# Optimization experiments

Hardware: AMD Instinct MI355X
Metric: run time of the kernel (lower is better)

The kernel has to match this reference:

```python
import jax, jax.numpy as jnp
import numpy as np

N_NODES, N_EDGES, HID = 30000, 480000, 128
N_GRAPHS, N_CLASSES = 128, 6
BN_EPS, ADD_SCORE = 1e-5, 0.5


def setup_inputs():
    key = jax.random.key(0)
    ks = jax.random.split(key, 12)
    g = lambda i, shape: jax.random.normal(ks[i], shape, jnp.float32) * 0.05
    return dict(
        x=jax.random.normal(ks[0], (N_NODES, HID), jnp.float32),
        edge_index=jax.random.randint(ks[1], (2, N_EDGES), 0, N_NODES, jnp.int32),
        batch=jnp.sort(jax.random.randint(ks[2], (N_NODES,), 0, N_GRAPHS, jnp.int32)),
        Wl=g(3, (6, HID, HID)), bl=jnp.zeros((6, HID), jnp.float32),
        Wr=g(4, (6, HID, HID)),
        gamma=jnp.ones((6, HID), jnp.float32), beta=jnp.zeros((6, HID), jnp.float32),
        Wlin=g(5, (3, HID, 2 * HID)), blin=jnp.zeros((3, HID), jnp.float32),
        Wp=g(6, (3, 2 * HID)), bp=jnp.zeros((3,), jnp.float32),
        Wf1=g(7, (HID, HID)), bf1=jnp.zeros((HID,), jnp.float32),
        Wf2=g(8, (N_CLASSES, HID)), bf2=jnp.zeros((N_CLASSES,), jnp.float32),
    )


def _sage(x, src, dst, emf, Wl_i, bl_i, Wr_i, N):
    # PyG SAGEConv: lin_l(mean_{j->i} x_j) + lin_r(x_i); emf masks dead edges
    msg = x[src] * emf[:, None]                              # [E,H]
    s = jax.ops.segment_sum(msg, dst, num_segments=N)
    c = jax.ops.segment_sum(emf, dst, num_segments=N)
    mean = s / jnp.maximum(c, 1.0)[:, None]
    return mean @ Wl_i.T + bl_i + x @ Wr_i.T


def _bn(x, g, b, nvf):
    # training-mode BatchNorm over valid (non-merged-away) nodes only
    cnt = jnp.maximum(nvf.sum(), 1.0)
    mu = (x * nvf[:, None]).sum(0) / cnt
    var = (((x - mu) ** 2) * nvf[:, None]).sum(0) / cnt
    return g * (x - mu) * jax.lax.rsqrt(var + BN_EPS) + b


def _edge_pool(x, src, dst, emb, nvb, Wp_i, bp_i, N, E):
    h = x.shape[1]
    # raw edge score = Linear(cat(x[src], x[dst]))
    raw = (x @ Wp_i[:h])[src] + (x @ Wp_i[h:])[dst] + bp_i   # [E]
    neg = jnp.finfo(x.dtype).min
    mx = jax.ops.segment_max(jnp.where(emb, raw, neg), dst, num_segments=N)
    z = jnp.where(emb, jnp.exp(jnp.where(emb, raw - mx[dst], 0.0)), 0.0)
    den = jax.ops.segment_sum(z, dst, num_segments=N)
    score = z / jnp.maximum(den, 1e-16)[dst] + ADD_SCORE     # softmax per dst + 0.5

    # greedy edge matching in descending score order (sequential, int-only carry)
    order = jnp.argsort(-jnp.where(emb, jax.lax.stop_gradient(score), -jnp.inf))

    def step(carry, i):
        matched, cluster, chosen = carry
        s, t = src[i], dst[i]
        ok = emb[i] & (~matched[s]) & (~matched[t]) & (s != t)
        rep, oth = jnp.minimum(s, t), jnp.maximum(s, t)
        matched = matched.at[s].set(matched[s] | ok)
        matched = matched.at[t].set(matched[t] | ok)
        cluster = cluster.at[oth].set(jnp.where(ok, rep, cluster[oth]))
        chosen = chosen.at[rep].set(jnp.where(ok, i, chosen[rep]))
        return (matched, cluster, chosen), None

    init = (~nvb, jnp.arange(N, dtype=jnp.int32), jnp.full((N,), -1, jnp.int32))
    (matched, cluster, chosen), _ = jax.lax.scan(step, init, order)

    # merged node = (x_s + x_t) * score(chosen edge); singleton score = 1
    nscore = jnp.where(chosen >= 0, score[jnp.maximum(chosen, 0)], 1.0)
    new_x = jax.ops.segment_sum(x, cluster, num_segments=N) * nscore[:, None]
    nvb2 = nvb & (cluster == jnp.arange(N, dtype=jnp.int32))
    # remap edges to cluster representatives; coalesce duplicates (self-loops kept, as PyG)
    key = jnp.where(emb, cluster[src] * N + cluster[dst], -1)  # N*N < 2**31
    uk = jnp.unique(key, size=E, fill_value=-1)
    emb2 = uk >= 0
    ukc = jnp.maximum(uk, 0)
    return new_x, ukc // N, ukc % N, emb2, nvb2


def reference(x, edge_index, batch, Wl, bl, Wr, gamma, beta, Wlin, blin, Wp, bp, Wf1, bf1, Wf2, bf2):
    N, E = x.shape[0], edge_index.shape[1]
    src, dst = edge_index[0], edge_index[1]
    emb = jnp.ones((E,), bool)   # edge-valid mask (fixed-shape graph coarsening)
    nvb = jnp.ones((N,), bool)   # node-valid mask
    for blk in range(3):
        emf, nvf = emb.astype(x.dtype), nvb.astype(x.dtype)
        i = 2 * blk
        h = _bn(jax.nn.relu(_sage(x, src, dst, emf, Wl[i], bl[i], Wr[i], N)), gamma[i], beta[i], nvf)
        h2 = _bn(jax.nn.relu(_sage(h, src, dst, emf, Wl[i + 1], bl[i + 1], Wr[i + 1], N)), gamma[i + 1], beta[i + 1], nvf)
        x = jnp.concatenate([h2, h], axis=1) @ Wlin[blk].T + blin[blk]  # dropout = identity (eval)
        x, src, dst, emb, nvb = _edge_pool(x, src, dst, emb, nvb, Wp[blk], bp[blk], N, E)
    nvf = nvb.astype(x.dtype)
    sums = jax.ops.segment_sum(x * nvf[:, None], batch, num_segments=N_GRAPHS)
    cnt = jax.ops.segment_sum(nvf, batch, num_segments=N_GRAPHS)
    pooled = sums / jnp.maximum(cnt, 1.0)[:, None]           # global_mean_pool
    hfc = jax.nn.relu(pooled @ Wf1.T + bf1)
    return jax.nn.log_softmax(hfc @ Wf2.T + bf2, axis=1)
```

## Files before the change

kernel.cpp:

```cpp
#include <hip/hip_runtime.h>
#include <stdint.h>

#define NN 30000
#define NE 480000
#define HID 128
#define NG 128
#define NC 6
#define BN_EPS 1e-5f
#define WPB 938
#define SLOTS 4

typedef unsigned int u32;
typedef unsigned long long u64;

__device__ __forceinline__ u64 ent_key(int4 ent) {
  return ((u64)(u32)ent.y << 32) | (u32)ent.x;
}

__global__ void k_init(const int* __restrict__ ei, int* srcA, int* dstA, int* nvb,
                       int* scal, int* b3, int* i2, float* gbuf) {
  int t = blockIdx.x * 256 + threadIdx.x;
  if (t < NE) { srcA[t] = ei[t]; dstA[t] = ei[NE + t]; }
  if (t < NN) nvb[t] = 1;
  if (t < 2 * NN) { b3[t] = 0; i2[t] = 0; }
  if (t < NG * HID + NG) gbuf[t] = 0.f;
  if (t == 0) { scal[0] = NE; scal[1] = 0; }
}

__global__ void k_csr_count(const int* __restrict__ pE, const int* __restrict__ src,
                            const int* __restrict__ dst, int* __restrict__ cnt,
                            int* __restrict__ icnt, const int* __restrict__ nvb,
                            int* __restrict__ pcnt) {
  int t = blockIdx.x * 256 + threadIdx.x;
  if (t < NN && nvb[t]) atomicAdd(pcnt, 1);
  if (t < *pE) {
    int s = src[t], d = dst[t];
    atomicAdd(&cnt[d], 1);
    if (s != d) { atomicAdd(&icnt[s], 1); atomicAdd(&icnt[d], 1); }
  }
}

__global__ __launch_bounds__(1024) void k_scan2(const int* __restrict__ in0, int* __restrict__ out0,
                                                const int* __restrict__ in1, int* __restrict__ out1) {
  const int* in = blockIdx.x ? in1 : in0;
  int* out = blockIdx.x ? out1 : out0;
  __shared__ int part[1024];
  int t = threadIdx.x;
  int chunk = (NN + 1023) / 1024;
  int b = t * chunk, e = b + chunk;
  if (b > NN) b = NN;
  if (e > NN) e = NN;
  int s = 0;
  for (int i = b; i < e; i++) s += in[i];
  part[t] = s;
  __syncthreads();
  for (int off = 1; off < 1024; off <<= 1) {
    int v = (t >= off) ? part[t - off] : 0;
    __syncthreads();
    part[t] += v;
    __syncthreads();
  }
  int excl = (t == 0) ? 0 : part[t - 1];
  for (int i = b; i < e; i++) { out[i] = excl; excl += in[i]; }
  if (t == 0) out[NN] = part[1023];
}

__global__ void k_csr_scatter(const int* __restrict__ pE, const int* __restrict__ dst,
                              const int* __restrict__ coff, int* __restrict__ cursor,
                              int* __restrict__ eids) {
  int e = blockIdx.x * 256 + threadIdx.x;
  if (e >= *pE) return;
  int d = dst[e];
  int pos = coff[d] + atomicAdd(&cursor[d], 1);
  eids[pos] = e;
}

__global__ __launch_bounds__(256) void k_sage_gather(
    const int* __restrict__ coff, const int* __restrict__ eids,
    const int* __restrict__ src, const float* __restrict__ x,
    float* __restrict__ mean) {
  int grp = threadIdx.x >> 5;
  int lane = threadIdx.x & 31;
  int n = blockIdx.x * 8 + grp;
  if (n >= NN) return;
  int b = coff[n], e2 = coff[n + 1];
  float4 acc = make_float4(0.f, 0.f, 0.f, 0.f);
  for (int i = b; i < e2; i++) {
    int s = src[eids[i]];
    float4 v = *(const float4*)(x + (size_t)s * HID + lane * 4);
    acc.x += v.x; acc.y += v.y; acc.z += v.z; acc.w += v.w;
  }
  float inv = 1.0f / fmaxf((float)(e2 - b), 1.0f);
  acc.x *= inv; acc.y *= inv; acc.z *= inv; acc.w *= inv;
  *(float4*)(mean + (size_t)n * HID + lane * 4) = acc;
}

__global__ __launch_bounds__(256) void gemm_dual(
    const float* __restrict__ A1, const float* __restrict__ W1,
    const float* __restrict__ A2, const float* __restrict__ W2,
    const float* __restrict__ bias, float* __restrict__ out,
    int M, int ldw, int relu, double* __restrict__ bnsum) {
  if (blockIdx.x == 0 && threadIdx.x < 2 * HID) bnsum[threadIdx.x] = 0.0;
  __shared__ float As[64][33];
  __shared__ float Ws[32][132];
  int row0 = blockIdx.x * 64;
  int tid = threadIdx.x;
  int cid = tid & 31;
  int rid = tid >> 5;
  float acc[8][4];
#pragma unroll
  for (int r = 0; r < 8; r++)
#pragma unroll
    for (int c = 0; c < 4; c++) acc[r][c] = 0.f;

  for (int srcI = 0; srcI < 2; ++srcI) {
    const float* A = srcI ? A2 : A1;
    const float* W = srcI ? W2 : W1;
    for (int kc = 0; kc < 128; kc += 32) {
#pragma unroll
      for (int i = 0; i < 2; ++i) {
        int idx = tid + i * 256;
        int r = idx >> 3;
        int c4 = (idx & 7) << 2;
        int gr = row0 + r;
        float4 v = make_float4(0.f, 0.f, 0.f, 0.f);
        if (gr < M) v = *(const float4*)(A + (size_t)gr * 128 + kc + c4);
        As[r][c4 + 0] = v.x; As[r][c4 + 1] = v.y; As[r][c4 + 2] = v.z; As[r][c4 + 3] = v.w;
      }
#pragma unroll
      for (int i = 0; i < 4; ++i) {
        int idx = tid + i * 256;
        int j = idx >> 3;
        int c4 = (idx & 7) << 2;
        float4 v = *(const float4*)(W + (size_t)j * ldw + kc + c4);
        Ws[c4 + 0][j] = v.x; Ws[c4 + 1][j] = v.y; Ws[c4 + 2][j] = v.z; Ws[c4 + 3][j] = v.w;
      }
      __syncthreads();
#pragma unroll
      for (int kk = 0; kk < 32; ++kk) {
        float4 w = *(const float4*)(&Ws[kk][cid * 4]);
#pragma unroll
        for (int r = 0; r < 8; ++r) {
          float a = As[rid * 8 + r][kk];
          acc[r][0] += a * w.x; acc[r][1] += a * w.y; acc[r][2] += a * w.z; acc[r][3] += a * w.w;
        }
      }
      __syncthreads();
    }
  }
#pragma unroll
  for (int r = 0; r < 8; ++r) {
    int gr = row0 + rid * 8 + r;
    if (gr >= M) continue;
#pragma unroll
    for (int c = 0; c < 4; ++c) {
      float v = acc[r][c] + bias[cid * 4 + c];
      if (relu) v = fmaxf(v, 0.f);
      out[(size_t)gr * 128 + cid * 4 + c] = v;
    }
  }
}

__global__ __launch_bounds__(128) void k_bn_stats(const float* __restrict__ x,
                                                  const int* __restrict__ nvb,
                                                  double* __restrict__ sums) {
  int k = threadIdx.x;
  int n0 = blockIdx.x * 64;
  float s = 0.f, q = 0.f;
  for (int r = 0; r < 64; r++) {
    int n = n0 + r;
    if (n >= NN) break;
    if (!nvb[n]) continue;
    float v = x[(size_t)n * HID + k];
    s += v; q += v * v;
  }
  atomicAdd(&sums[k], (double)s);
  atomicAdd(&sums[HID + k], (double)q);
}

__global__ void k_bn_apply(float* __restrict__ x, const double* __restrict__ sums,
                           const int* __restrict__ cnt, const float* __restrict__ gamma,
                           const float* __restrict__ beta) {
  int t = blockIdx.x * 256 + threadIdx.x;
  if (t >= NN * HID) return;
  int k = t & 127;
  double c = (double)((*cnt > 1) ? *cnt : 1);
  double mu = sums[k] / c;
  double var = sums[HID + k] / c - mu * mu;
  if (var < 0.0) var = 0.0;
  float inv = (float)(1.0 / sqrt(var + (double)BN_EPS));
  x[t] = gamma[k] * (x[t] - (float)mu) * inv + beta[k];
}

__global__ void k_node_proj(const float* __restrict__ x, const float* __restrict__ Wp,
                            float* __restrict__ px1, float* __restrict__ px2) {
  int n = blockIdx.x * 256 + threadIdx.x;
  if (n >= NN) return;
  const float* xr = x + (size_t)n * HID;
  float s1 = 0.f, s2 = 0.f;
#pragma unroll 8
  for (int k = 0; k < HID; k += 4) {
    float4 v = *(const float4*)(xr + k);
    float4 w1 = *(const float4*)(Wp + k);
    float4 w2 = *(const float4*)(Wp + HID + k);
    s1 += v.x * w1.x + v.y * w1.y + v.z * w1.z + v.w * w1.w;
    s2 += v.x * w2.x + v.y * w2.y + v.z * w2.z + v.w * w2.w;
  }
  px1[n] = s1; px2[n] = s2;
}

__global__ void k_edge_softmax_seed(
    const int* __restrict__ coff, const int* __restrict__ eids,
    const int* __restrict__ src, const float* __restrict__ px1,
    const float* __restrict__ px2, const float* __restrict__ bp,
    float* __restrict__ score, u64* __restrict__ ekey, u64* __restrict__ S) {
  int n = blockIdx.x * 256 + threadIdx.x;
  if (n >= NN) return;
  S[n] = 0ull;
  int b = coff[n], e2 = coff[n + 1];
  if (b == e2) return;
  float p2 = px2[n] + *bp;
  float mx = -3.4e38f;
  for (int i = b; i < e2; i++) {
    float r = px1[src[eids[i]]] + p2;
    mx = fmaxf(mx, r);
  }
  double den = 0.0;
  for (int i = b; i < e2; i++) {
    int eid = eids[i];
    float z = expf(px1[src[eid]] + p2 - mx);
    score[eid] = z;
    den += (double)z;
  }
  if (den < 1e-16) den = 1e-16;
  double invd = 1.0 / den;
  for (int i = b; i < e2; i++) {
    int eid = eids[i];
    float sc = (float)((double)score[eid] * invd) + 0.5f;
    score[eid] = sc;
    ekey[eid] = ((u64)__float_as_uint(sc) << 32) | (u64)(0xFFFFFFFFu - (u32)eid);
  }
}

__global__ void k_inc_scatter(const int* __restrict__ pE, const int* __restrict__ src,
                              const int* __restrict__ dst, const u64* __restrict__ ekey,
                              const int* __restrict__ ioff, int* __restrict__ icur,
                              int4* __restrict__ ielist) {
  int e = blockIdx.x * 256 + threadIdx.x;
  if (e >= *pE) return;
  int s = src[e], d = dst[e];
  if (s == d) return;
  u64 k = ekey[e];
  int4 ent;
  ent.x = (int)(u32)(k & 0xFFFFFFFFull);
  ent.y = (int)(u32)(k >> 32);
  ent.w = 0;
  ent.z = d;
  ielist[ioff[s] + atomicAdd(&icur[s], 1)] = ent;
  ent.z = s;
  ielist[ioff[d] + atomicAdd(&icur[d], 1)] = ent;
}

__global__ __launch_bounds__(256) void k_suitor(
    const int* __restrict__ ioff, const int4* __restrict__ ielist,
    const int* __restrict__ src, const int* __restrict__ dst,
    u64* __restrict__ S) {
  int wid = threadIdx.x >> 6;
  int lane = threadIdx.x & 63;
  int n = blockIdx.x * 4 + wid;
  if (n >= NN) return;
  int cur = n;
  while (cur >= 0) {
    int b = ioff[cur], e2 = ioff[cur + 1];
    int deg = e2 - b;
    if (deg == 0) break;
    if (deg <= 64 * SLOTS) {
      u64 key[SLOTS]; int pv[SLOTS];
#pragma unroll
      for (int s = 0; s < SLOTS; s++) {
        key[s] = 0; pv[s] = 0;
        int i = b + s * 64 + lane;
        if (i < e2) {
          int4 ent = ielist[i];
          key[s] = ent_key(ent);
          pv[s] = ent.z;
        }
      }
      long long res;
      for (;;) {
        u64 localBest = 0;
#pragma unroll
        for (int s = 0; s < SLOTS; s++) {
          if (!key[s]) continue;
          u64 sv = __hip_atomic_load(&S[pv[s]], __ATOMIC_RELAXED, __HIP_MEMORY_SCOPE_AGENT);
          if (sv >= key[s]) key[s] = 0;
          else if (key[s] > localBest) localBest = key[s];
        }
        u64 bestKey = localBest;
#pragma unroll
        for (int o = 32; o > 0; o >>= 1) {
          u64 other = __shfl_xor(bestKey, o, 64);
          if (other > bestKey) bestKey = other;
        }
        if (bestKey == 0) { res = -1; break; }
        int ms = -1;
#pragma unroll
        for (int s = 0; s < SLOTS; s++)
          if (ms < 0 && key[s] == bestKey) ms = s;
        u64 ball = __ballot(ms >= 0);
        int owner = (int)(__ffsll((long long)ball) - 1);
        long long r0 = -3;
        if (lane == owner) {
          int bv = pv[ms];
          u64 old = atomicMax(&S[bv], bestKey);
          if (old >= bestKey) { key[ms] = 0; r0 = -2; }
          else if (old == 0) r0 = -1;
          else {
            int eo = (int)(0xFFFFFFFFu - (u32)(old & 0xFFFFFFFFull));
            int so = src[eo], do_ = dst[eo];
            r0 = (so == bv) ? do_ : so;
          }
        }
        res = __shfl(r0, owner, 64);
        if (res != -2) break;
      }
      if (res < 0) break;
      cur = (int)res;
    } else {
      u64 bestKey = 0;
      for (int i = b + lane; i < e2; i += 64) {
        int4 ent = ielist[i];
        u64 k = ent_key(ent);
        if (k <= bestKey) continue;
        u64 sv = __hip_atomic_load(&S[ent.z], __ATOMIC_RELAXED, __HIP_MEMORY_SCOPE_AGENT);
        if (k > sv) bestKey = k;
      }
#pragma unroll
      for (int o = 32; o > 0; o >>= 1) {
        u64 other = __shfl_xor(bestKey, o, 64);
        if (other > bestKey) bestKey = other;
      }
      long long r0 = -1;
      if (bestKey != 0 && lane == 0) {
        int e = (int)(0xFFFFFFFFu - (u32)(bestKey & 0xFFFFFFFFull));
        int es = src[e], ed = dst[e];
        int bv = (es == cur) ? ed : es;
        u64 old = atomicMax(&S[bv], bestKey);
        if (old >= bestKey) r0 = cur;
        else if (old != 0) {
          int eo = (int)(0xFFFFFFFFu - (u32)(old & 0xFFFFFFFFull));
          int so = src[eo], do_ = dst[eo];
          r0 = (so == bv) ? do_ : so;
        }
      }
      long long res = (bestKey != 0) ? __shfl(r0, 0, 64) : -1;
      cur = (int)res;
    }
  }
}

__global__ __launch_bounds__(256) void k_new_x(
    const u64* __restrict__ S, const int* __restrict__ src, const int* __restrict__ dst,
    const float* __restrict__ score, const float* __restrict__ x,
    float* __restrict__ out, int* __restrict__ cluster,
    int* __restrict__ nvb, int* __restrict__ b3zero) {
  int gt = blockIdx.x * 256 + threadIdx.x;
  if (gt < 2 * NN) b3zero[gt] = 0;
  int grp = threadIdx.x >> 5;
  int lane = threadIdx.x & 31;
  int n = blockIdx.x * 8 + grp;
  if (n >= NN) return;
  u64 k = S[n];
  int partner = -1;
  int rep = n;
  bool isOth = false;
  float sc = 1.f;
  if (k) {
    int e = (int)(0xFFFFFFFFu - (u32)(k & 0xFFFFFFFFull));
    int s = src[e], d = dst[e];
    int other = (s == n) ? d : s;
    if (S[other] == k) {
      if (n > other) { isOth = true; rep = other; }
      else { partner = other; sc = score[e]; }
    }
  }
  float4 v = make_float4(0.f, 0.f, 0.f, 0.f);
  if (!isOth) {
    v = *(const float4*)(x + (size_t)n * HID + lane * 4);
    if (partner >= 0) {
      float4 w = *(const float4*)(x + (size_t)partner * HID + lane * 4);
      v.x = (v.x + w.x) * sc; v.y = (v.y + w.y) * sc;
      v.z = (v.z + w.z) * sc; v.w = (v.w + w.w) * sc;
    }
  }
  *(float4*)(out + (size_t)n * HID + lane * 4) = v;
  if (lane == 0) {
    cluster[n] = rep;
    nvb[n] = (nvb[n] && !isOth) ? 1 : 0;
  }
}

__global__ void k_bucket_count(const int* __restrict__ pE, const int* __restrict__ src,
                               const int* __restrict__ cluster, int* __restrict__ bcount) {
  int e = blockIdx.x * 256 + threadIdx.x;
  if (e >= *pE) return;
  atomicAdd(&bcount[cluster[src[e]]], 1);
}

__global__ __launch_bounds__(1024) void k_scan(const int* __restrict__ in, int* __restrict__ out,
                                               int n, int* totalDst) {
  __shared__ int part[1024];
  int t = threadIdx.x;
  int chunk = (n + 1023) / 1024;
  int b = t * chunk, e = b + chunk;
  if (b > n) b = n;
  if (e > n) e = n;
  int s = 0;
  for (int i = b; i < e; i++) s += in[i];
  part[t] = s;
  __syncthreads();
  for (int off = 1; off < 1024; off <<= 1) {
    int v = (t >= off) ? part[t - off] : 0;
    __syncthreads();
    part[t] += v;
    __syncthreads();
  }
  int excl = (t == 0) ? 0 : part[t - 1];
  int total = part[1023];
  for (int i = b; i < e; i++) { out[i] = excl; excl += in[i]; }
  if (t == 0) {
    out[n] = total;
    if (totalDst) *totalDst = total;
  }
}

__global__ void k_bucket_scatter(const int* __restrict__ pE, const int* __restrict__ src,
                                 const int* __restrict__ dst, const int* __restrict__ cluster,
                                 const int* __restrict__ boffs, int* __restrict__ bcursor,
                                 int* __restrict__ bucket) {
  int e = blockIdx.x * 256 + threadIdx.x;
  if (e >= *pE) return;
  int cs = cluster[src[e]], cd = cluster[dst[e]];
  int pos = boffs[cs] + atomicAdd(&bcursor[cs], 1);
  bucket[pos] = cd;
}

__global__ __launch_bounds__(256) void k_dedup_bitmap(
    const int* __restrict__ boffs, int* __restrict__ bucket,
    int* __restrict__ ucount) {
  __shared__ u32 bm[4][960];
  int wid = threadIdx.x >> 6;
  int lane = threadIdx.x & 63;
  int n = blockIdx.x * 4 + wid;
  int b = boffs[n], e = boffs[n + 1];
  for (int w = lane; w < 960; w += 64) bm[wid][w] = 0;
  __syncthreads();
  for (int i = b + lane; i < e; i += 64)
    atomicOr(&bm[wid][bucket[i] >> 5], 1u << (bucket[i] & 31));
  __syncthreads();
  int w0 = lane * 15;
  int w1 = w0 + 15; if (w1 > WPB) w1 = WPB;
  int cnt = 0;
  for (int w = w0; w < w1; w++) cnt += __popc(bm[wid][w]);
  int inc = cnt;
  for (int o = 1; o < 64; o <<= 1) { int v = __shfl_up(inc, o); if (lane >= o) inc += v; }
  int excl = inc - cnt;
  int total = __shfl(inc, 63);
  int pos = b + excl;
  for (int w = w0; w < w1; w++) {
    u32 v = bm[wid][w];
    while (v) { int bit = __ffs(v) - 1; bucket[pos++] = (w << 5) | bit; v &= v - 1; }
  }
  if (lane == 0) ucount[n] = total;
}

__global__ void k_emit(const int* __restrict__ boffs, const int* __restrict__ bucket,
                       const int* __restrict__ bucount, const int* __restrict__ bnoffs,
                       int* __restrict__ srcO, int* __restrict__ dstO,
                       int* __restrict__ b3zero, int* __restrict__ i2zero,
                       int* __restrict__ pcnt) {
  int t = blockIdx.x * 256 + threadIdx.x;
  int stride = gridDim.x * 256;
  for (int z = t; z < 2 * NN; z += stride) { b3zero[z] = 0; i2zero[z] = 0; }
  if (t == 0) *pcnt = 0;
  if (t >= NN) return;
  int u = bucount[t], b = boffs[t], o = bnoffs[t];
  for (int i = 0; i < u; i++) { srcO[o + i] = t; dstO[o + i] = bucket[b + i]; }
}

__global__ void k_graph_pool(const int* __restrict__ nvb, const int* __restrict__ batch,
                             const float* __restrict__ x, float* __restrict__ gsum,
                             float* __restrict__ gcnt) {
  int t = blockIdx.x * 256 + threadIdx.x;
  int n = t >> 2;
  if (n >= NN) return;
  if (!nvb[n]) return;
  int sub = t & 3;
  int g = batch[n];
  const float* xr = x + (size_t)n * HID + sub * 32;
  float* o = gsum + (size_t)g * HID + sub * 32;
#pragma unroll
  for (int i = 0; i < 8; i++) {
    float4 v = *(const float4*)(xr + i * 4);
    atomicAdd(o + i * 4 + 0, v.x); atomicAdd(o + i * 4 + 1, v.y);
    atomicAdd(o + i * 4 + 2, v.z); atomicAdd(o + i * 4 + 3, v.w);
  }
  if (sub == 0) atomicAdd(&gcnt[g], 1.0f);
}

__global__ __launch_bounds__(128) void k_head1(const float* __restrict__ gsum,
                                               const float* __restrict__ gcnt,
                                               const float* __restrict__ Wf1,
                                               const float* __restrict__ bf1,
                                               float* __restrict__ hfc) {
  int g = blockIdx.x;
  int j = threadIdx.x;
  __shared__ float p[HID];
  float c = fmaxf(gcnt[g], 1.f);
  p[j] = gsum[g * HID + j] / c;
  __syncthreads();
  float s = bf1[j];
  const float* w = Wf1 + (size_t)j * HID;
  for (int k = 0; k < HID; k++) s += p[k] * w[k];
  hfc[g * HID + j] = fmaxf(s, 0.f);
}

__global__ void k_head2(const float* __restrict__ hfc, const float* __restrict__ Wf2,
                        const float* __restrict__ bf2, float* __restrict__ out) {
  int g = blockIdx.x;
  int t = threadIdx.x;
  __shared__ float lg[NC];
  if (t < NC) {
    float s = bf2[t];
    const float* w = Wf2 + (size_t)t * HID;
    const float* h = hfc + (size_t)g * HID;
    for (int k = 0; k < HID; k++) s += h[k] * w[k];
    lg[t] = s;
  }
  __syncthreads();
  if (t == 0) {
    float m = lg[0];
    for (int c = 1; c < NC; c++) m = fmaxf(m, lg[c]);
    float se = 0.f;
    for (int c = 0; c < NC; c++) se += expf(lg[c] - m);
    float lse = m + logf(se);
    for (int c = 0; c < NC; c++) out[g * NC + c] = lg[c] - lse;
  }
}

extern "C" void kernel_launch(void* const* d_in, const int* in_sizes, int n_in,
                              void* d_out, int out_size, void* d_ws, size_t ws_size,
                              hipStream_t stream) {
  const float* x0 = (const float*)d_in[0];
  const int* ei = (const int*)d_in[1];
  const int* batch = (const int*)d_in[2];
  const float* Wl = (const float*)d_in[3];
  const float* bl = (const float*)d_in[4];
  const float* Wr = (const float*)d_in[5];
  const float* gamma = (const float*)d_in[6];
  const float* beta = (const float*)d_in[7];
  const float* Wlin = (const float*)d_in[8];
  const float* blin = (const float*)d_in[9];
  const float* Wp = (const float*)d_in[10];
  const float* bp = (const float*)d_in[11];
  const float* Wf1 = (const float*)d_in[12];
  const float* bf1 = (const float*)d_in[13];
  const float* Wf2 = (const float*)d_in[14];
  const float* bf2 = (const float*)d_in[15];
  float* out = (float*)d_out;

  const int NH = NN * HID;
  size_t off = 0;
  char* base = (char*)d_ws;
  auto carve = [&](size_t bytes) -> char* {
    char* p = base + off;
    off += (bytes + 255) & ~(size_t)255;
    return p;
  };
  float* xa = (float*)carve((size_t)NH * 4);
  float* xb = (float*)carve((size_t)NH * 4);
  float* xc = (float*)carve((size_t)NH * 4);
  float* xd = (float*)carve((size_t)NH * 4);
  int* srcA = (int*)carve((size_t)NE * 4);
  int* dstA = (int*)carve((size_t)NE * 4);
  int* srcB = (int*)carve((size_t)NE * 4);
  int* dstB = (int*)carve((size_t)NE * 4);
  float* escore = (float*)carve((size_t)NE * 4);
  int* ebucket = (int*)carve((size_t)NE * 4);
  int* eids = (int*)carve((size_t)NE * 4);
  u64* ekey = (u64*)carve((size_t)NE * 8);
  u64* S = (u64*)carve((size_t)NN * 8);
  float* npx1 = (float*)carve((size_t)NN * 4);
  float* npx2 = (float*)carve((size_t)NN * 4);
  int* ncluster = (int*)carve((size_t)NN * 4);
  int* nvb = (int*)carve((size_t)NN * 4);
  int* b3 = (int*)carve((size_t)3 * NN * 4);
  int* bcount = b3;
  int* bcursor = b3 + NN;
  int* bucount = b3 + 2 * NN;
  int* i2 = (int*)carve((size_t)2 * NN * 4);
  int* icnt = i2;
  int* icursor = i2 + NN;
  int* boffs = (int*)carve((size_t)(NN + 1) * 4);
  int* bnoffs = (int*)carve((size_t)(NN + 1) * 4);
  int* csroff = (int*)carve((size_t)(NN + 1) * 4);
  int* ioff = (int*)carve((size_t)(NN + 1) * 4);
  double* bnsum = (double*)carve((size_t)2 * HID * 8);
  float* gbuf = (float*)carve((size_t)(NG * HID + NG) * 4);
  float* gsum = gbuf;
  float* gcnt = gbuf + NG * HID;
  float* ghfc = (float*)carve((size_t)NG * HID * 4);
  int* scal = (int*)carve(64 * 4);
  (void)ws_size; (void)n_in; (void)in_sizes; (void)out_size;

  int4* ielist = (int4*)xc;

  int* pE = scal;
  int* pcnt = scal + 1;

  hipMemcpyAsync(xa, x0, (size_t)NH * 4, hipMemcpyDeviceToDevice, stream);
  k_init<<<1875, 256, 0, stream>>>(ei, srcA, dstA, nvb, scal, b3, i2, gbuf);

  int* srcC = srcA; int* dstC = dstA; int* srcN = srcB; int* dstN = dstB;
  float* xcur = xa;
  float* xtmp = xd;

  auto sage = [&](const float* xin, float* xout, int L) {
    k_sage_gather<<<3750, 256, 0, stream>>>(csroff, eids, srcC, xin, xtmp);
    gemm_dual<<<469, 256, 0, stream>>>(xtmp, Wl + (size_t)L * HID * HID, xin,
                                       Wr + (size_t)L * HID * HID, bl + (size_t)L * HID,
                                       xout, NN, HID, 1, bnsum);
    k_bn_stats<<<469, 128, 0, stream>>>(xout, nvb, bnsum);
    k_bn_apply<<<15000, 256, 0, stream>>>(xout, bnsum, pcnt, gamma + (size_t)L * HID,
                                          beta + (size_t)L * HID);
  };

  for (int b = 0; b < 3; b++) {
    k_csr_count<<<1875, 256, 0, stream>>>(pE, srcC, dstC, bcount, icnt, nvb, pcnt);
    k_scan2<<<2, 1024, 0, stream>>>(bcount, csroff, icnt, ioff);
    k_csr_scatter<<<1875, 256, 0, stream>>>(pE, dstC, csroff, bcursor, eids);

    sage(xcur, xb, 2 * b);
    sage(xb, xc, 2 * b + 1);
    gemm_dual<<<469, 256, 0, stream>>>(xc, Wlin + (size_t)b * HID * 2 * HID, xb,
                                       Wlin + (size_t)b * HID * 2 * HID + HID,
                                       blin + (size_t)b * HID, xcur, NN, 2 * HID, 0, bnsum);

    k_node_proj<<<118, 256, 0, stream>>>(xcur, Wp + (size_t)b * 2 * HID, npx1, npx2);
    k_edge_softmax_seed<<<118, 256, 0, stream>>>(csroff, eids, srcC, npx1, npx2, bp + b,
                                                 escore, ekey, S);
    k_inc_scatter<<<1875, 256, 0, stream>>>(pE, srcC, dstC, ekey, ioff, icursor, ielist);
    k_suitor<<<7500, 256, 0, stream>>>(ioff, ielist, srcC, dstC, S);
    k_new_x<<<3750, 256, 0, stream>>>(S, srcC, dstC, escore, xcur, xtmp,
                                      ncluster, nvb, b3);

    if (b < 2) {
      k_bucket_count<<<1875, 256, 0, stream>>>(pE, srcC, ncluster, bcount);
      k_scan<<<1, 1024, 0, stream>>>(bcount, boffs, NN, (int*)nullptr);
      k_bucket_scatter<<<1875, 256, 0, stream>>>(pE, srcC, dstC, ncluster, boffs, bcursor,
                                                 ebucket);
      k_dedup_bitmap<<<7500, 256, 0, stream>>>(boffs, ebucket, bucount);
      k_scan<<<1, 1024, 0, stream>>>(bucount, bnoffs, NN, pE);
      k_emit<<<235, 256, 0, stream>>>(boffs, ebucket, bucount, bnoffs, srcN, dstN,
                                      b3, i2, pcnt);
      { int* t = srcC; srcC = srcN; srcN = t; t = dstC; dstC = dstN; dstN = t; }
    }
    { float* t = xcur; xcur = xtmp; xtmp = t; }
  }

  k_graph_pool<<<469, 256, 0, stream>>>(nvb, batch, xcur, gsum, gcnt);
  k_head1<<<NG, 128, 0, stream>>>(gsum, gcnt, Wf1, bf1, ghfc);
  k_head2<<<NG, 32, 0, stream>>>(ghfc, Wf2, bf2, out);
}
```

Baseline: 2.843 ms.

## Fuse BN stats into 128x128 GEMM, pre-gather CSR sources, drop input copy

The GEMM is retiled to 128-row blocks with an 8x8 register tile per thread. It now accumulates per-column batch-norm sums in its epilogue, so the separate stats kernel is gone. The CSR scatter also writes source node ids in CSR order, which removes the eids indirection in the SAGE gather and the edge softmax; the gather is unrolled by two. The initial device-to-device copy of x is replaced by reading the input directly in the first block. These changes cut kernel launches and memory passes, at the cost of more register pressure in the GEMM and fewer blocks launched.

```diff
diff --git a/kernel.cpp b/kernel.cpp
--- a/kernel.cpp
+++ b/kernel.cpp
@@ -9,6 +9,7 @@
 #define BN_EPS 1e-5f
 #define WPB 938
 #define SLOTS 4
+#define GPAD 132
 
 typedef unsigned int u32;
 typedef unsigned long long u64;
@@ -65,117 +66,131 @@
   if (t == 0) out[NN] = part[1023];
 }
 
-__global__ void k_csr_scatter(const int* __restrict__ pE, const int* __restrict__ dst,
-                              const int* __restrict__ coff, int* __restrict__ cursor,
-                              int* __restrict__ eids) {
+__global__ void k_csr_scatter(const int* __restrict__ pE, const int* __restrict__ src,
+                              const int* __restrict__ dst, const int* __restrict__ coff,
+                              int* __restrict__ cursor, int* __restrict__ eids,
+                              int* __restrict__ gsrc) {
   int e = blockIdx.x * 256 + threadIdx.x;
   if (e >= *pE) return;
   int d = dst[e];
   int pos = coff[d] + atomicAdd(&cursor[d], 1);
   eids[pos] = e;
+  gsrc[pos] = src[e];
 }
 
 __global__ __launch_bounds__(256) void k_sage_gather(
-    const int* __restrict__ coff, const int* __restrict__ eids,
-    const int* __restrict__ src, const float* __restrict__ x,
-    float* __restrict__ mean) {
+    const int* __restrict__ coff, const int* __restrict__ gsrc,
+    const float* __restrict__ x, float* __restrict__ mean,
+    double* __restrict__ bnsum) {
+  if (blockIdx.x == 0 && threadIdx.x < 2 * HID) bnsum[threadIdx.x] = 0.0;
   int grp = threadIdx.x >> 5;
   int lane = threadIdx.x & 31;
   int n = blockIdx.x * 8 + grp;
   if (n >= NN) return;
   int b = coff[n], e2 = coff[n + 1];
   float4 acc = make_float4(0.f, 0.f, 0.f, 0.f);
-  for (int i = b; i < e2; i++) {
-    int s = src[eids[i]];
-    float4 v = *(const float4*)(x + (size_t)s * HID + lane * 4);
-    acc.x += v.x; acc.y += v.y; acc.z += v.z; acc.w += v.w;
+  int i = b;
+  for (; i + 1 < e2; i += 2) {
+    int s0 = gsrc[i], s1 = gsrc[i + 1];
+    float4 v0 = *(const float4*)(x + (size_t)s0 * HID + lane * 4);
+    float4 v1 = *(const float4*)(x + (size_t)s1 * HID + lane * 4);
+    acc.x += v0.x; acc.y += v0.y; acc.z += v0.z; acc.w += v0.w;
+    acc.x += v1.x; acc.y += v1.y; acc.z += v1.z; acc.w += v1.w;
+  }
+  if (i < e2) {
+    int s0 = gsrc[i];
+    float4 v0 = *(const float4*)(x + (size_t)s0 * HID + lane * 4);
+    acc.x += v0.x; acc.y += v0.y; acc.z += v0.z; acc.w += v0.w;
   }
   float inv = 1.0f / fmaxf((float)(e2 - b), 1.0f);
   acc.x *= inv; acc.y *= inv; acc.z *= inv; acc.w *= inv;
   *(float4*)(mean + (size_t)n * HID + lane * 4) = acc;
 }
 
-__global__ __launch_bounds__(256) void gemm_dual(
+__global__ __launch_bounds__(256) void gemm_dual2(
     const float* __restrict__ A1, const float* __restrict__ W1,
     const float* __restrict__ A2, const float* __restrict__ W2,
     const float* __restrict__ bias, float* __restrict__ out,
-    int M, int ldw, int relu, double* __restrict__ bnsum) {
-  if (blockIdx.x == 0 && threadIdx.x < 2 * HID) bnsum[threadIdx.x] = 0.0;
-  __shared__ float As[64][33];
-  __shared__ float Ws[32][132];
-  int row0 = blockIdx.x * 64;
+    int M, int ldw, int relu, const int* __restrict__ nvb,
+    double* __restrict__ bnsum, int dostats) {
+  __shared__ float Ast[16][GPAD];
+  __shared__ float Ws[16][GPAD];
   int tid = threadIdx.x;
-  int cid = tid & 31;
-  int rid = tid >> 5;
-  float acc[8][4];
-#pragma unroll
-  for (int r = 0; r < 8; r++)
-#pragma unroll
-    for (int c = 0; c < 4; c++) acc[r][c] = 0.f;
-
-  for (int srcI = 0; srcI < 2; ++srcI) {
+  int rg = tid >> 4, cg = tid & 15;
+  int r0 = rg * 8, c0 = cg * 8;
+  int row0 = blockIdx.x * 128;
+  float acc[8][8];
+#pragma unroll
+  for (int a = 0; a < 8; a++)
+#pragma unroll
+    for (int bq = 0; bq < 8; bq++) acc[a][bq] = 0.f;
+
+  for (int srcI = 0; srcI < 2; srcI++) {
     const float* A = srcI ? A2 : A1;
     const float* W = srcI ? W2 : W1;
-    for (int kc = 0; kc < 128; kc += 32) {
-#pragma unroll
-      for (int i = 0; i < 2; ++i) {
-        int idx = tid + i * 256;
-        int r = idx >> 3;
-        int c4 = (idx & 7) << 2;
+    for (int kc = 0; kc < 128; kc += 16) {
+#pragma unroll
+      for (int i = 0; i < 2; i++) {
+        int k = tid + i * 256;
+        int r = k >> 2, c4 = (k & 3) << 2;
         int gr = row0 + r;
         float4 v = make_float4(0.f, 0.f, 0.f, 0.f);
         if (gr < M) v = *(const float4*)(A + (size_t)gr * 128 + kc + c4);
-        As[r][c4 + 0] = v.x; As[r][c4 + 1] = v.y; As[r][c4 + 2] = v.z; As[r][c4 + 3] = v.w;
-      }
-#pragma unroll
-      for (int i = 0; i < 4; ++i) {
-        int idx = tid + i * 256;
-        int j = idx >> 3;
-        int c4 = (idx & 7) << 2;
-        float4 v = *(const float4*)(W + (size_t)j * ldw + kc + c4);
-        Ws[c4 + 0][j] = v.x; Ws[c4 + 1][j] = v.y; Ws[c4 + 2][j] = v.z; Ws[c4 + 3][j] = v.w;
+        Ast[c4 + 0][r] = v.x; Ast[c4 + 1][r] = v.y;
+        Ast[c4 + 2][r] = v.z; Ast[c4 + 3][r] = v.w;
+        float4 w = *(const float4*)(W + (size_t)r * ldw + kc + c4);
+        Ws[c4 + 0][r] = w.x; Ws[c4 + 1][r] = w.y;
+        Ws[c4 + 2][r] = w.z; Ws[c4 + 3][r] = w.w;
       }
       __syncthreads();
 #pragma unroll
-      for (int kk = 0; kk < 32; ++kk) {
-        float4 w = *(const float4*)(&Ws[kk][cid * 4]);
-#pragma unroll
-        for (int r = 0; r < 8; ++r) {
-          float a = As[rid * 8 + r][kk];
-          acc[r][0] += a * w.x; acc[r][1] += a * w.y; acc[r][2] += a * w.z; acc[r][3] += a * w.w;
-        }
+      for (int kk = 0; kk < 16; kk++) {
+        float4 a0 = *(const float4*)(&Ast[kk][r0]);
+        float4 a1 = *(const float4*)(&Ast[kk][r0 + 4]);
+        float4 b0 = *(const float4*)(&Ws[kk][c0]);
+        float4 b1 = *(const float4*)(&Ws[kk][c0 + 4]);
+        float av[8] = {a0.x, a0.y, a0.z, a0.w, a1.x, a1.y, a1.z, a1.w};
+        float bv[8] = {b0.x, b0.y, b0.z, b0.w, b1.x, b1.y, b1.z, b1.w};
+#pragma unroll
+        for (int rr = 0; rr < 8; rr++)
+#pragma unroll
+          for (int cc = 0; cc < 8; cc++) acc[rr][cc] += av[rr] * bv[cc];
       }
       __syncthreads();
     }
   }
-#pragma unroll
-  for (int r = 0; r < 8; ++r) {
-    int gr = row0 + rid * 8 + r;
+
+  float sCol[8], qCol[8];
+#pragma unroll
+  for (int cc = 0; cc < 8; cc++) { sCol[cc] = 0.f; qCol[cc] = 0.f; }
+#pragma unroll
+  for (int rr = 0; rr < 8; rr++) {
+    int gr = row0 + r0 + rr;
     if (gr >= M) continue;
-#pragma unroll
-    for (int c = 0; c < 4; ++c) {
-      float v = acc[r][c] + bias[cid * 4 + c];
+    int valid = dostats ? nvb[gr] : 0;
+    float vv[8];
+#pragma unroll
+    for (int cc = 0; cc < 8; cc++) {
+      float v = acc[rr][cc] + bias[c0 + cc];
       if (relu) v = fmaxf(v, 0.f);
-      out[(size_t)gr * 128 + cid * 4 + c] = v;
+      vv[cc] = v;
+      if (valid) { sCol[cc] += v; qCol[cc] += v * v; }
     }
-  }
-}
-
-__global__ __launch_bounds__(128) void k_bn_stats(const float* __restrict__ x,
-                                                  const int* __restrict__ nvb,
-                                                  double* __restrict__ sums) {
-  int k = threadIdx.x;
-  int n0 = blockIdx.x * 64;
-  float s = 0.f, q = 0.f;
-  for (int r = 0; r < 64; r++) {
-    int n = n0 + r;
-    if (n >= NN) break;
-    if (!nvb[n]) continue;
-    float v = x[(size_t)n * HID + k];
-    s += v; q += v * v;
-  }
-  atomicAdd(&sums[k], (double)s);
-  atomicAdd(&sums[HID + k], (double)q);
+    *(float4*)(out + (size_t)gr * 128 + c0) = make_float4(vv[0], vv[1], vv[2], vv[3]);
+    *(float4*)(out + (size_t)gr * 128 + c0 + 4) = make_float4(vv[4], vv[5], vv[6], vv[7]);
+  }
+  if (dostats) {
+#pragma unroll
+    for (int cc = 0; cc < 8; cc++) { Ast[rg][c0 + cc] = sCol[cc]; Ws[rg][c0 + cc] = qCol[cc]; }
+    __syncthreads();
+    if (tid < HID) {
+      float s = 0.f, q = 0.f;
+#pragma unroll
+      for (int g = 0; g < 16; g++) { s += Ast[g][tid]; q += Ws[g][tid]; }
+      atomicAdd(&bnsum[tid], (double)s);
+      atomicAdd(&bnsum[HID + tid], (double)q);
+    }
+  }
 }
 
 __global__ void k_bn_apply(float* __restrict__ x, const double* __restrict__ sums,
@@ -211,7 +226,7 @@
 
 __global__ void k_edge_softmax_seed(
     const int* __restrict__ coff, const int* __restrict__ eids,
-    const int* __restrict__ src, const float* __restrict__ px1,
+    const int* __restrict__ gsrc, const float* __restrict__ px1,
     const float* __restrict__ px2, const float* __restrict__ bp,
     float* __restrict__ score, u64* __restrict__ ekey, u64* __restrict__ S) {
   int n = blockIdx.x * 256 + threadIdx.x;
@@ -222,13 +237,13 @@
   float p2 = px2[n] + *bp;
   float mx = -3.4e38f;
   for (int i = b; i < e2; i++) {
-    float r = px1[src[eids[i]]] + p2;
+    float r = px1[gsrc[i]] + p2;
     mx = fmaxf(mx, r);
   }
   double den = 0.0;
   for (int i = b; i < e2; i++) {
     int eid = eids[i];
-    float z = expf(px1[src[eid]] + p2 - mx);
+    float z = expf(px1[gsrc[i]] + p2 - mx);
     score[eid] = z;
     den += (double)z;
   }
@@ -588,6 +603,7 @@
   float* escore = (float*)carve((size_t)NE * 4);
   int* ebucket = (int*)carve((size_t)NE * 4);
   int* eids = (int*)carve((size_t)NE * 4);
+  int* gsrc = (int*)carve((size_t)NE * 4);
   u64* ekey = (u64*)carve((size_t)NE * 8);
   u64* S = (u64*)carve((size_t)NN * 8);
   float* npx1 = (float*)carve((size_t)NN * 4);
@@ -618,7 +634,6 @@
   int* pE = scal;
   int* pcnt = scal + 1;
 
-  hipMemcpyAsync(xa, x0, (size_t)NH * 4, hipMemcpyDeviceToDevice, stream);
   k_init<<<1875, 256, 0, stream>>>(ei, srcA, dstA, nvb, scal, b3, i2, gbuf);
 
   int* srcC = srcA; int* dstC = dstA; int* srcN = srcB; int* dstN = dstB;
@@ -626,28 +641,30 @@
   float* xtmp = xd;
 
   auto sage = [&](const float* xin, float* xout, int L) {
-    k_sage_gather<<<3750, 256, 0, stream>>>(csroff, eids, srcC, xin, xtmp);
-    gemm_dual<<<469, 256, 0, stream>>>(xtmp, Wl + (size_t)L * HID * HID, xin,
-                                       Wr + (size_t)L * HID * HID, bl + (size_t)L * HID,
-                                       xout, NN, HID, 1, bnsum);
-    k_bn_stats<<<469, 128, 0, stream>>>(xout, nvb, bnsum);
+    k_sage_gather<<<3750, 256, 0, stream>>>(csroff, gsrc, xin, xtmp, bnsum);
+    gemm_dual2<<<235, 256, 0, stream>>>(xtmp, Wl + (size_t)L * HID * HID, xin,
+                                        Wr + (size_t)L * HID * HID, bl + (size_t)L * HID,
+                                        xout, NN, HID, 1, nvb, bnsum, 1);
     k_bn_apply<<<15000, 256, 0, stream>>>(xout, bnsum, pcnt, gamma + (size_t)L * HID,
                                           beta + (size_t)L * HID);
   };
 
   for (int b = 0; b < 3; b++) {
+    const float* xin = (b == 0) ? x0 : (const float*)xcur;
+
     k_csr_count<<<1875, 256, 0, stream>>>(pE, srcC, dstC, bcount, icnt, nvb, pcnt);
     k_scan2<<<2, 1024, 0, stream>>>(bcount, csroff, icnt, ioff);
-    k_csr_scatter<<<1875, 256, 0, stream>>>(pE, dstC, csroff, bcursor, eids);
-
-    sage(xcur, xb, 2 * b);
+    k_csr_scatter<<<1875, 256, 0, stream>>>(pE, srcC, dstC, csroff, bcursor, eids, gsrc);
+
+    sage(xin, xb, 2 * b);
     sage(xb, xc, 2 * b + 1);
-    gemm_dual<<<469, 256, 0, stream>>>(xc, Wlin + (size_t)b * HID * 2 * HID, xb,
-                                       Wlin + (size_t)b * HID * 2 * HID + HID,
-                                       blin + (size_t)b * HID, xcur, NN, 2 * HID, 0, bnsum);
+    gemm_dual2<<<235, 256, 0, stream>>>(xc, Wlin + (size_t)b * HID * 2 * HID, xb,
+                                        Wlin + (size_t)b * HID * 2 * HID + HID,
+                                        blin + (size_t)b * HID, xcur, NN, 2 * HID, 0,
+                                        nvb, bnsum, 0);
 
     k_node_proj<<<118, 256, 0, stream>>>(xcur, Wp + (size_t)b * 2 * HID, npx1, npx2);
-    k_edge_softmax_seed<<<118, 256, 0, stream>>>(csroff, eids, srcC, npx1, npx2, bp + b,
+    k_edge_softmax_seed<<<118, 256, 0, stream>>>(csroff, eids, gsrc, npx1, npx2, bp + b,
                                                  escore, ekey, S);
     k_inc_scatter<<<1875, 256, 0, stream>>>(pE, srcC, dstC, ekey, ioff, icursor, ielist);
     k_suitor<<<7500, 256, 0, stream>>>(ioff, ielist, srcC, dstC, S);
```

Result: faster. 2.544 ms (-10.5%).
